# Performance work log

Measured on AMD Instinct MI355X. Metric: run time of the kernel, lower is better.

Reference implementation:

```python
import jax, jax.numpy as jnp
import numpy as np

B, NDOC, L, E = 32, 4, 512, 512
SCALE = np.float32(1.0 / np.sqrt(E))
NEG_INF = np.float32(-1e9)


def setup_inputs() -> dict:
    key = jax.random.key(0)
    k1, k2, k3, k4, k5, k6 = jax.random.split(key, 6)
    return {
        "x1": jax.random.normal(k1, (B, L, E), dtype=jnp.float32),
        "x2": jax.random.normal(k2, (B, NDOC, L, E), dtype=jnp.float32),
        "x1_len": jax.random.randint(k3, (B,), 0, L, dtype=jnp.int64),
        "x2_len": jax.random.randint(k4, (B, NDOC), 0, L, dtype=jnp.int64),
        "fusion_w": jax.random.normal(k5, (2 * E, E), dtype=jnp.float32) * 0.02,
        "fusion_b": jnp.zeros((E,), dtype=jnp.float32),
        "out_w": jax.random.normal(k6, (8 * E, 2 * E), dtype=jnp.float32) * 0.02,
        "out_b": jnp.zeros((2 * E,), dtype=jnp.float32),
    }


def reference(x1, x2, x1_len, x2_len, fusion_w, fusion_b, out_w, out_b):
    # Faithful to torch .repeat(1,4,...): concatenate 4 full copies along batch,
    # so attention row i pairs x1[i % B] with x2[i // 4, i % 4].
    x1_rep = jnp.tile(x1, (NDOC, 1, 1))          # [4B, L, E]
    x2_r = x2.reshape(-1, L, E)                  # [4B, L, E]

    x1_len_r = jnp.tile(x1_len, NDOC)            # [4B] (same tiling as x1_rep)
    x2_len_r = x2_len.reshape(-1)                # [4B]
    pos = jnp.arange(L)
    q_mask = pos[None, :] < x1_len_r[:, None]    # [4B, L]
    k_mask = pos[None, :] < x2_len_r[:, None]    # [4B, L]
    mask = q_mask[:, :, None] & k_mask[:, None, :]  # [4B, L, L]

    # scaled-dot-product attention with masked_fill(mask==0, -1e9)
    scores = jnp.einsum('bqe,bke->bqk', x1_rep, x2_r) * SCALE  # [4B, L, L]
    scores = jnp.where(mask, scores, NEG_INF)
    attn = jax.nn.softmax(scores, axis=-1)
    x1_att = jnp.einsum('bqk,bke->bqe', attn, x2_r)            # [4B, L, E]

    cat = jnp.concatenate([x1_rep - x1_att, x1_rep * x1_att], axis=-1)  # [4B, L, 2E]
    fus = jax.nn.relu(cat @ fusion_w + fusion_b)                        # [4B, L, E]

    x1_mean = jnp.mean(fus, axis=1)              # [4B, E]
    x1_max = jnp.max(fus, axis=1)                # [4B, E]
    pooled = jnp.concatenate([x1_mean.reshape(B, -1), x1_max.reshape(B, -1)], axis=-1)  # [B, 8E]
    out = jax.nn.relu(pooled @ out_w + out_b)    # [B, 2E]
    return out, attn
```

## Files before the change

kernel.cpp:

```cpp
#include <hip/hip_runtime.h>
#include <cstddef>

#define BATCH 32
#define NB    128
#define LL    512
#define EE    512
#define SCALE 0.044194173824159216f
#define NEG_INF -1e9f

typedef __attribute__((ext_vector_type(4))) float f32x4;
typedef __attribute__((ext_vector_type(8))) short s16x8;
typedef __attribute__((ext_vector_type(4))) unsigned short u16x4;

#define STEP_FENCE() asm volatile("s_waitcnt vmcnt(0) lgkmcnt(0)\n\ts_barrier" ::: "memory")

__device__ __forceinline__ unsigned short f2b(float f) {
    unsigned u = __float_as_uint(f);
    u += 0x7FFFu + ((u >> 16) & 1u);
    return (unsigned short)(u >> 16);
}
__device__ __forceinline__ float b2f(unsigned short h) {
    return __uint_as_float(((unsigned)h) << 16);
}

__device__ __forceinline__ void gld_lds16(const unsigned short* g, unsigned short* l) {
    __builtin_amdgcn_global_load_lds(
        (const __attribute__((address_space(1))) void*)g,
        (__attribute__((address_space(3))) void*)l, 16, 0, 0);
}

__global__ __launch_bounds__(256) void k_cvt_x1(
    const float* __restrict__ x1, unsigned short* __restrict__ x1bf)
{
    const size_t idx = (size_t)blockIdx.x * 256 + threadIdx.x;
    f32x4 v = *(const f32x4*)(x1 + idx * 4);
    u16x4 o = { f2b(v[0]), f2b(v[1]), f2b(v[2]), f2b(v[3]) };
    *(u16x4*)(x1bf + idx * 4) = o;
}

__global__ __launch_bounds__(256) void k_cvt_x2(
    const float* __restrict__ x2,
    unsigned short* __restrict__ x2bf, unsigned short* __restrict__ x2t)
{
    __shared__ float T[64][65];
    const int i = blockIdx.z, kb = blockIdx.y * 64, eb = blockIdx.x * 64;
    const float* src = x2 + (size_t)i * LL * EE;
    unsigned short* db = x2bf + (size_t)i * LL * EE;
    unsigned short* dt = x2t  + (size_t)i * LL * EE;
    const int t = threadIdx.x, r16 = t >> 4, c4 = (t & 15) * 4;
#pragma unroll
    for (int p = 0; p < 4; ++p) {
        int row = p * 16 + r16;
        f32x4 v = *(const f32x4*)(src + (size_t)(kb + row) * EE + eb + c4);
        T[row][c4] = v[0]; T[row][c4+1] = v[1]; T[row][c4+2] = v[2]; T[row][c4+3] = v[3];
        u16x4 o = { f2b(v[0]), f2b(v[1]), f2b(v[2]), f2b(v[3]) };
        *(u16x4*)(db + (size_t)(kb + row) * EE + eb + c4) = o;
    }
    __syncthreads();
#pragma unroll
    for (int p = 0; p < 4; ++p) {
        int erow = p * 16 + r16;
        u16x4 o = { f2b(T[c4][erow]), f2b(T[c4+1][erow]),
                    f2b(T[c4+2][erow]), f2b(T[c4+3][erow]) };
        *(u16x4*)(dt + (size_t)(eb + erow) * LL + kb + c4) = o;
    }
}

__global__ __launch_bounds__(256) void k_cvt_fw(
    const float* __restrict__ fw, unsigned short* __restrict__ fwt)
{
    __shared__ float T[64][65];
    const int jb = blockIdx.y * 64, eb = blockIdx.x * 64;
    const int t = threadIdx.x, r16 = t >> 4, c4 = (t & 15) * 4;
#pragma unroll
    for (int p = 0; p < 4; ++p) {
        int row = p * 16 + r16;
        f32x4 v = *(const f32x4*)(fw + (size_t)(jb + row) * EE + eb + c4);
        T[row][c4] = v[0]; T[row][c4+1] = v[1]; T[row][c4+2] = v[2]; T[row][c4+3] = v[3];
    }
    __syncthreads();
#pragma unroll
    for (int p = 0; p < 4; ++p) {
        int erow = p * 16 + r16;
#pragma unroll
        for (int k = 0; k < 4; ++k) {
            int jold = jb + c4 + k;
            int jn = (jold < 512) ? (2 * jold) : (2 * (jold - 512) + 1);
            fwt[(size_t)(eb + erow) * 1024 + jn] = f2b(T[c4 + k][erow]);
        }
    }
}

__global__ __launch_bounds__(1024, 4) void k_attn(
    const unsigned short* __restrict__ x1bf,
    const unsigned short* __restrict__ x2bf,
    const unsigned short* __restrict__ x2t,
    const int* __restrict__ x1_len, const int* __restrict__ x2_len,
    float* __restrict__ attn, unsigned short* __restrict__ Cbuf)
{
    __shared__ __align__(16) char smem[163840];
    unsigned short* Ast0 = (unsigned short*)smem;
    unsigned short* Ast1 = (unsigned short*)(smem + 8192);
    unsigned short* Bst0 = (unsigned short*)(smem + 16384);
    unsigned short* Bst1 = (unsigned short*)(smem + 49152);
    float* rowred = (float*)(smem + 131072);
    float* rowst  = (float*)(smem + 131072 + 4096);
    unsigned short* Vst0 = (unsigned short*)(smem + 131072);
    unsigned short* Vst1 = (unsigned short*)(smem + 147456);

    const int flat = blockIdx.x + blockIdx.y * 128;
    const int xcd  = flat & 7;
    const int idx  = flat >> 3;
    const int i    = xcd * 16 + (idx >> 2);
    const int q0   = (idx & 3) * 128;
    const unsigned short* Ag = x1bf + (size_t)(i & 31) * LL * EE;
    const unsigned short* Bg = x2bf + (size_t)i * LL * EE;
    const unsigned short* Vg = x2t  + (size_t)i * LL * EE;
    const int t = threadIdx.x, lane = t & 63;
    const int w = t >> 6;
    const int m = lane & 15, quad = lane >> 4;
    const int lrow = lane >> 2, lcol = (lane & 3) * 8;
    const int wrow = w >> 3, wcol = w & 7;

    f32x4 acc[4][4];
#pragma unroll
    for (int r = 0; r < 4; ++r)
#pragma unroll
        for (int c = 0; c < 4; ++c) acc[r][c] = (f32x4){0.f, 0.f, 0.f, 0.f};

    if (w < 8)
        gld_lds16(Ag + (size_t)(q0 + w * 16 + lrow) * EE + lcol, &Ast0[w * 512]);
    gld_lds16(Bg + (size_t)((2 * w) * 16 + lrow) * EE + lcol, &Bst0[(2 * w) * 512]);
    gld_lds16(Bg + (size_t)((2 * w + 1) * 16 + lrow) * EE + lcol, &Bst0[(2 * w + 1) * 512]);
    STEP_FENCE();

    for (int it = 0; it < 16; ++it) {
        unsigned short* Ac = (it & 1) ? Ast1 : Ast0;
        unsigned short* Bc = (it & 1) ? Bst1 : Bst0;
        if (it < 15) {
            unsigned short* An = (it & 1) ? Ast0 : Ast1;
            unsigned short* Bn = (it & 1) ? Bst0 : Bst1;
            const int e0n = (it + 1) * 32;
            if (w < 8)
                gld_lds16(Ag + (size_t)(q0 + w * 16 + lrow) * EE + e0n + lcol, &An[w * 512]);
            gld_lds16(Bg + (size_t)((2 * w) * 16 + lrow) * EE + e0n + lcol, &Bn[(2 * w) * 512]);
            gld_lds16(Bg + (size_t)((2 * w + 1) * 16 + lrow) * EE + e0n + lcol, &Bn[(2 * w + 1) * 512]);
        }
        s16x8 af[4], bfr[4];
#pragma unroll
        for (int rt = 0; rt < 4; ++rt)
            af[rt] = *(const s16x8*)&Ac[(wrow * 64 + rt * 16 + m) * 32 + quad * 8];
#pragma unroll
        for (int ct = 0; ct < 4; ++ct)
            bfr[ct] = *(const s16x8*)&Bc[(wcol * 64 + ct * 16 + m) * 32 + quad * 8];
#pragma unroll
        for (int rt = 0; rt < 4; ++rt)
#pragma unroll
            for (int ct = 0; ct < 4; ++ct)
                acc[rt][ct] = __builtin_amdgcn_mfma_f32_16x16x32_bf16(
                    af[rt], bfr[ct], acc[rt][ct], 0, 0, 0);
        STEP_FENCE();
    }

    const int qlen = x1_len[i & 31];
    const int klen = x2_len[i];

#pragma unroll
    for (int rt = 0; rt < 4; ++rt)
#pragma unroll
        for (int reg = 0; reg < 4; ++reg) {
            const int l = q0 + wrow * 64 + rt * 16 + quad * 4 + reg;
            const bool qok = l < qlen;
#pragma unroll
            for (int ct = 0; ct < 4; ++ct) {
                const int k = wcol * 64 + ct * 16 + m;
                acc[rt][ct][reg] = (qok && k < klen) ? acc[rt][ct][reg] * SCALE : NEG_INF;
            }
        }

#pragma unroll
    for (int rt = 0; rt < 4; ++rt)
#pragma unroll
        for (int reg = 0; reg < 4; ++reg) {
            float v = fmaxf(fmaxf(acc[rt][0][reg], acc[rt][1][reg]),
                            fmaxf(acc[rt][2][reg], acc[rt][3][reg]));
            v = fmaxf(v, __shfl_xor(v, 1));
            v = fmaxf(v, __shfl_xor(v, 2));
            v = fmaxf(v, __shfl_xor(v, 4));
            v = fmaxf(v, __shfl_xor(v, 8));
            if (m == 0)
                rowred[wcol * 128 + wrow * 64 + rt * 16 + quad * 4 + reg] = v;
        }
    __syncthreads();
    if (t < 128) {
        float mx = rowred[t];
#pragma unroll
        for (int c = 1; c < 8; ++c) mx = fmaxf(mx, rowred[c * 128 + t]);
        rowst[t] = mx;
    }
    __syncthreads();

#pragma unroll
    for (int rt = 0; rt < 4; ++rt)
#pragma unroll
        for (int reg = 0; reg < 4; ++reg) {
            const int lloc = wrow * 64 + rt * 16 + quad * 4 + reg;
            const float mx = rowst[lloc];
            float s = 0.f;
#pragma unroll
            for (int ct = 0; ct < 4; ++ct) {
                float p = __expf(acc[rt][ct][reg] - mx);
                acc[rt][ct][reg] = p;
                s += p;
            }
            s += __shfl_xor(s, 1);
            s += __shfl_xor(s, 2);
            s += __shfl_xor(s, 4);
            s += __shfl_xor(s, 8);
            if (m == 0) rowred[wcol * 128 + lloc] = s;
        }
    __syncthreads();
    if (t < 128) {
        float s = 0.f;
#pragma unroll
        for (int c = 0; c < 8; ++c) s += rowred[c * 128 + t];
        rowst[t] = 1.0f / s;
    }
    __syncthreads();

    float* op = attn + (size_t)i * LL * LL;
#pragma unroll
    for (int rt = 0; rt < 4; ++rt)
#pragma unroll
        for (int reg = 0; reg < 4; ++reg) {
            const int lloc = wrow * 64 + rt * 16 + quad * 4 + reg;
            const float inv = rowst[lloc];
#pragma unroll
            for (int ct = 0; ct < 4; ++ct) {
                const int k = wcol * 64 + ct * 16 + m;
                float p = acc[rt][ct][reg] * inv;
                op[(size_t)(q0 + lloc) * LL + k] = p;
                unsigned off = (unsigned)(lloc * 1024 + k * 2) ^ (unsigned)((lloc & 7) << 4);
                *(unsigned short*)(smem + off) = f2b(p);
            }
        }
    __syncthreads();

    const int pwr = w >> 2, pwc = w & 3;
    unsigned short* Cb = Cbuf + (size_t)i * LL * 1024;
#pragma unroll
    for (int eh = 0; eh < 2; ++eh) {
        f32x4 acc2[2][4];
#pragma unroll
        for (int r = 0; r < 2; ++r)
#pragma unroll
            for (int c = 0; c < 4; ++c) acc2[r][c] = (f32x4){0.f, 0.f, 0.f, 0.f};

        gld_lds16(Vg + (size_t)(eh * 256 + w * 16 + lrow) * LL + lcol, &Vst0[w * 512]);
        STEP_FENCE();

        for (int kt = 0; kt < 16; ++kt) {
            const int k0 = kt * 32;
            unsigned short* Vc = (kt & 1) ? Vst1 : Vst0;
            if (kt < 15) {
                unsigned short* Vn = (kt & 1) ? Vst0 : Vst1;
                gld_lds16(Vg + (size_t)(eh * 256 + w * 16 + lrow) * LL + k0 + 32 + lcol,
                          &Vn[w * 512]);
            }
            s16x8 paf[2], pbf[4];
#pragma unroll
            for (int rt = 0; rt < 2; ++rt) {
                const int lr = pwr * 32 + rt * 16 + m;
                unsigned off = (unsigned)(lr * 1024 + (k0 + quad * 8) * 2)
                               ^ (unsigned)((lr & 7) << 4);
                paf[rt] = *(const s16x8*)(smem + off);
            }
#pragma unroll
            for (int ct = 0; ct < 4; ++ct)
                pbf[ct] = *(const s16x8*)&Vc[(pwc * 64 + ct * 16 + m) * 32 + quad * 8];
#pragma unroll
            for (int rt = 0; rt < 2; ++rt)
#pragma unroll
                for (int ct = 0; ct < 4; ++ct)
                    acc2[rt][ct] = __builtin_amdgcn_mfma_f32_16x16x32_bf16(
                        paf[rt], pbf[ct], acc2[rt][ct], 0, 0, 0);
            STEP_FENCE();
        }

#pragma unroll
        for (int rt = 0; rt < 2; ++rt)
#pragma unroll
            for (int reg = 0; reg < 4; ++reg) {
                const int l = q0 + pwr * 32 + rt * 16 + quad * 4 + reg;
#pragma unroll
                for (int ct = 0; ct < 4; ++ct) {
                    const int e = eh * 256 + pwc * 64 + ct * 16 + m;
                    float att = acc2[rt][ct][reg];
                    float xv  = b2f(Ag[(size_t)l * EE + e]);
                    unsigned pr = (unsigned)f2b(xv - att) | ((unsigned)f2b(xv * att) << 16);
                    *(unsigned*)(Cb + (size_t)l * 1024 + 2 * e) = pr;
                }
            }
    }
}

__global__ __launch_bounds__(256) void k_fuse_mfma(
    const unsigned short* __restrict__ Cbuf,
    const unsigned short* __restrict__ fwt,
    const float* __restrict__ fb,
    float* __restrict__ pmean, float* __restrict__ pmax)
{
    __shared__ unsigned short Al[128 * 32];
    __shared__ unsigned short Bl[128 * 32];
    __shared__ float psum[2][128];
    __shared__ float pmx[2][128];
    const int i  = blockIdx.x;
    const int lt = blockIdx.y >> 2;
    const int e0 = (blockIdx.y & 3) * 128;
    const unsigned short* Ab = Cbuf + ((size_t)i * LL + lt * 128) * 1024;
    const int t = threadIdx.x, lane = t & 63;
    const int w = t >> 6, wrow = w >> 1, wcol = w & 1;
    const int m = lane & 15, quad = lane >> 4;
    const int lrow = lane >> 2, lcol = (lane & 3) * 8;

    float bias[4];
#pragma unroll
    for (int ct = 0; ct < 4; ++ct) bias[ct] = fb[e0 + wcol * 64 + ct * 16 + m];
    float csum[4] = {0.f, 0.f, 0.f, 0.f};
    float cmax[4] = {-3e38f, -3e38f, -3e38f, -3e38f};

    f32x4 acc[4][4];
#pragma unroll
    for (int r = 0; r < 4; ++r)
#pragma unroll
        for (int c = 0; c < 4; ++c) acc[r][c] = (f32x4){0.f, 0.f, 0.f, 0.f};

    for (int j0 = 0; j0 < 1024; j0 += 32) {
#pragma unroll
        for (int c = 0; c < 2; ++c) {
            const int s = c * 4 + w;
            gld_lds16(Ab + (size_t)(s * 16 + lrow) * 1024 + j0 + lcol, &Al[s * 512]);
            gld_lds16(fwt + (size_t)(e0 + s * 16 + lrow) * 1024 + j0 + lcol, &Bl[s * 512]);
        }
        __syncthreads();
        s16x8 af[4], bfr[4];
#pragma unroll
        for (int rt = 0; rt < 4; ++rt)
            af[rt] = *(const s16x8*)&Al[(wrow * 64 + rt * 16 + m) * 32 + quad * 8];
#pragma unroll
        for (int ct = 0; ct < 4; ++ct)
            bfr[ct] = *(const s16x8*)&Bl[(wcol * 64 + ct * 16 + m) * 32 + quad * 8];
#pragma unroll
        for (int rt = 0; rt < 4; ++rt)
#pragma unroll
            for (int ct = 0; ct < 4; ++ct)
                acc[rt][ct] = __builtin_amdgcn_mfma_f32_16x16x32_bf16(
                    af[rt], bfr[ct], acc[rt][ct], 0, 0, 0);
        __syncthreads();
    }
#pragma unroll
    for (int rt = 0; rt < 4; ++rt)
#pragma unroll
        for (int reg = 0; reg < 4; ++reg)
#pragma unroll
            for (int ct = 0; ct < 4; ++ct) {
                float f = fmaxf(acc[rt][ct][reg] + bias[ct], 0.f);
                csum[ct] += f;
                cmax[ct] = fmaxf(cmax[ct], f);
            }
#pragma unroll
    for (int ct = 0; ct < 4; ++ct) {
        csum[ct] += __shfl_xor(csum[ct], 16);
        csum[ct] += __shfl_xor(csum[ct], 32);
        cmax[ct] = fmaxf(cmax[ct], __shfl_xor(cmax[ct], 16));
        cmax[ct] = fmaxf(cmax[ct], __shfl_xor(cmax[ct], 32));
    }
    if (quad == 0) {
#pragma unroll
        for (int ct = 0; ct < 4; ++ct) {
            psum[wrow][wcol * 64 + ct * 16 + m] = csum[ct];
            pmx[wrow][wcol * 64 + ct * 16 + m] = cmax[ct];
        }
    }
    __syncthreads();
    if (t < 128) {
        float s  = psum[0][t] + psum[1][t];
        float mx = fmaxf(pmx[0][t], pmx[1][t]);
        pmean[((size_t)i * 4 + lt) * EE + e0 + t] = s;
        pmax[((size_t)i * 4 + lt) * EE + e0 + t]  = mx;
    }
}

__global__ __launch_bounds__(256) void k_out_split(
    const float* __restrict__ pmean, const float* __restrict__ pmax,
    const float* __restrict__ ow, float* __restrict__ partial)
{
    __shared__ float ps[256];
    const int kc = blockIdx.x;
    const int b  = blockIdx.y;
    const int t  = threadIdx.x;
    const int j  = kc * 256 + t;
    const int jj = (j < 2048) ? j : j - 2048;
    const int ii = 4 * b + (jj >> 9);
    const int e  = jj & 511;
    float v;
    if (j < 2048) {
        const float* bp = pmean + (size_t)ii * 4 * EE + e;
        v = (bp[0] + bp[512] + bp[1024] + bp[1536]) * (1.0f / 512.0f);
    } else {
        const float* bp = pmax + (size_t)ii * 4 * EE + e;
        v = fmaxf(fmaxf(bp[0], bp[512]), fmaxf(bp[1024], bp[1536]));
    }
    ps[t] = v;
    __syncthreads();
    f32x4 acc = {0.f, 0.f, 0.f, 0.f};
    const float* wp = ow + (size_t)kc * 256 * 1024 + t * 4;
#pragma unroll 8
    for (int q = 0; q < 256; ++q) {
        f32x4 w4 = *(const f32x4*)(wp + (size_t)q * 1024);
        float p = ps[q];
        acc[0] = fmaf(p, w4[0], acc[0]);
        acc[1] = fmaf(p, w4[1], acc[1]);
        acc[2] = fmaf(p, w4[2], acc[2]);
        acc[3] = fmaf(p, w4[3], acc[3]);
    }
    *(f32x4*)(partial + ((size_t)kc * 32 + b) * 1024 + t * 4) = acc;
}

__global__ __launch_bounds__(256) void k_out_final(
    const float* __restrict__ partial, const float* __restrict__ ob,
    float* __restrict__ out)
{
    const int idx = blockIdx.x * 256 + threadIdx.x;
    const int b = idx >> 10, o = idx & 1023;
    float s = ob[o];
#pragma unroll
    for (int kc = 0; kc < 16; ++kc)
        s += partial[((size_t)kc * 32 + b) * 1024 + o];
    out[idx] = fmaxf(s, 0.f);
}

extern "C" void kernel_launch(void* const* d_in, const int* in_sizes, int n_in,
                              void* d_out, int out_size, void* d_ws, size_t ws_size,
                              hipStream_t stream)
{
    const float* x1     = (const float*)d_in[0];
    const float* x2     = (const float*)d_in[1];
    const int*   x1_len = (const int*)d_in[2];
    const int*   x2_len = (const int*)d_in[3];
    const float* fw     = (const float*)d_in[4];
    const float* fb     = (const float*)d_in[5];
    const float* ow     = (const float*)d_in[6];
    const float* ob     = (const float*)d_in[7];

    float* out  = (float*)d_out;
    float* attn = out + (size_t)BATCH * 1024;

    char* wp = (char*)d_ws;
    unsigned short* x1bf   = (unsigned short*)wp; wp += (size_t)BATCH * LL * EE * 2;
    unsigned short* x2bf   = (unsigned short*)wp; wp += (size_t)NB * LL * EE * 2;
    unsigned short* x2t    = (unsigned short*)wp; wp += (size_t)NB * LL * EE * 2;
    unsigned short* Cbuf   = (unsigned short*)wp; wp += (size_t)NB * LL * 1024 * 2;
    unsigned short* fwt    = (unsigned short*)wp; wp += (size_t)EE * 1024 * 2;
    float* pmean   = (float*)wp; wp += (size_t)NB * 4 * EE * 4;
    float* pmax    = (float*)wp; wp += (size_t)NB * 4 * EE * 4;
    float* partial = (float*)wp; wp += (size_t)16 * BATCH * 1024 * 4;

    k_cvt_x1<<<dim3(BATCH * LL * EE / 4 / 256), 256, 0, stream>>>(x1, x1bf);
    k_cvt_x2<<<dim3(8, 8, NB), 256, 0, stream>>>(x2, x2bf, x2t);
    k_cvt_fw<<<dim3(8, 16), 256, 0, stream>>>(fw, fwt);
    k_attn<<<dim3(128, 4), 1024, 0, stream>>>(x1bf, x2bf, x2t, x1_len, x2_len, attn, Cbuf);
    k_fuse_mfma<<<dim3(128, 16), 256, 0, stream>>>(Cbuf, fwt, fb, pmean, pmax);
    k_out_split<<<dim3(16, BATCH), 256, 0, stream>>>(pmean, pmax, ow, partial);
    k_out_final<<<dim3(BATCH * 1024 / 256), 256, 0, stream>>>(partial, ob, out);
}
```

Baseline: 576.7 us.

## Triple-buffer global-to-LDS staging in score and fusion GEMM loops

Replaces the double-buffered load/compute loops in the attention score GEMM and the fusion GEMM with a three-slot ring. Each step waits only for the oldest in-flight loads using partial vmcnt counts and a single barrier per iteration, with loads issued two steps ahead. This is meant to hide global-load latency and drop the second per-step barrier and full drain. In exchange it uses more LDS (three 40 KB slots in k_attn overlap the region later reused for row stats and V, and k_fuse grows to 48 KB). The correctness of the waits depends on the exact per-wave load counts.

```diff
diff --git a/kernel.cpp b/kernel.cpp
--- a/kernel.cpp
+++ b/kernel.cpp
@@ -99,10 +99,6 @@
     float* __restrict__ attn, unsigned short* __restrict__ Cbuf)
 {
     __shared__ __align__(16) char smem[163840];
-    unsigned short* Ast0 = (unsigned short*)smem;
-    unsigned short* Ast1 = (unsigned short*)(smem + 8192);
-    unsigned short* Bst0 = (unsigned short*)(smem + 16384);
-    unsigned short* Bst1 = (unsigned short*)(smem + 49152);
     float* rowred = (float*)(smem + 131072);
     float* rowst  = (float*)(smem + 131072 + 4096);
     unsigned short* Vst0 = (unsigned short*)(smem + 131072);
@@ -128,24 +124,30 @@
 #pragma unroll
         for (int c = 0; c < 4; ++c) acc[r][c] = (f32x4){0.f, 0.f, 0.f, 0.f};
 
-    if (w < 8)
-        gld_lds16(Ag + (size_t)(q0 + w * 16 + lrow) * EE + lcol, &Ast0[w * 512]);
-    gld_lds16(Bg + (size_t)((2 * w) * 16 + lrow) * EE + lcol, &Bst0[(2 * w) * 512]);
-    gld_lds16(Bg + (size_t)((2 * w + 1) * 16 + lrow) * EE + lcol, &Bst0[(2 * w + 1) * 512]);
-    STEP_FENCE();
-
+#define STAGE_SCORES(sl, base)                                                          \
+    do {                                                                                \
+        unsigned short* An_ = (unsigned short*)(base);                                  \
+        unsigned short* Bn_ = (unsigned short*)((char*)(base) + 8192);                  \
+        const int e0_ = (sl) * 32;                                                      \
+        if (w < 8)                                                                      \
+            gld_lds16(Ag + (size_t)(q0 + w * 16 + lrow) * EE + e0_ + lcol, &An_[w * 512]); \
+        gld_lds16(Bg + (size_t)((2 * w) * 16 + lrow) * EE + e0_ + lcol, &Bn_[(2 * w) * 512]); \
+        gld_lds16(Bg + (size_t)((2 * w + 1) * 16 + lrow) * EE + e0_ + lcol, &Bn_[(2 * w + 1) * 512]); \
+    } while (0)
+
+    STAGE_SCORES(0, smem);
+    STAGE_SCORES(1, smem + 40960);
+
+#pragma unroll
     for (int it = 0; it < 16; ++it) {
-        unsigned short* Ac = (it & 1) ? Ast1 : Ast0;
-        unsigned short* Bc = (it & 1) ? Bst1 : Bst0;
-        if (it < 15) {
-            unsigned short* An = (it & 1) ? Ast0 : Ast1;
-            unsigned short* Bn = (it & 1) ? Bst0 : Bst1;
-            const int e0n = (it + 1) * 32;
-            if (w < 8)
-                gld_lds16(Ag + (size_t)(q0 + w * 16 + lrow) * EE + e0n + lcol, &An[w * 512]);
-            gld_lds16(Bg + (size_t)((2 * w) * 16 + lrow) * EE + e0n + lcol, &Bn[(2 * w) * 512]);
-            gld_lds16(Bg + (size_t)((2 * w + 1) * 16 + lrow) * EE + e0n + lcol, &Bn[(2 * w + 1) * 512]);
-        }
+        if (it == 15)   asm volatile("s_waitcnt vmcnt(0)" ::: "memory");
+        else if (w < 8) asm volatile("s_waitcnt vmcnt(3)" ::: "memory");
+        else            asm volatile("s_waitcnt vmcnt(2)" ::: "memory");
+        __builtin_amdgcn_s_barrier();
+        if (it < 14) STAGE_SCORES(it + 2, smem + 40960 * ((it + 2) % 3));
+        char* cb = smem + 40960 * (it % 3);
+        unsigned short* Ac = (unsigned short*)cb;
+        unsigned short* Bc = (unsigned short*)(cb + 8192);
         s16x8 af[4], bfr[4];
 #pragma unroll
         for (int rt = 0; rt < 4; ++rt)
@@ -159,8 +161,8 @@
             for (int ct = 0; ct < 4; ++ct)
                 acc[rt][ct] = __builtin_amdgcn_mfma_f32_16x16x32_bf16(
                     af[rt], bfr[ct], acc[rt][ct], 0, 0, 0);
-        STEP_FENCE();
-    }
+    }
+    __syncthreads();
 
     const int qlen = x1_len[i & 31];
     const int klen = x2_len[i];
@@ -302,6 +304,7 @@
                 }
             }
     }
+#undef STAGE_SCORES
 }
 
 __global__ __launch_bounds__(256) void k_fuse_mfma(
@@ -310,8 +313,7 @@
     const float* __restrict__ fb,
     float* __restrict__ pmean, float* __restrict__ pmax)
 {
-    __shared__ unsigned short Al[128 * 32];
-    __shared__ unsigned short Bl[128 * 32];
+    __shared__ __align__(16) char fsm[49152];
     __shared__ float psum[2][128];
     __shared__ float pmx[2][128];
     const int i  = blockIdx.x;
@@ -335,29 +337,46 @@
 #pragma unroll
         for (int c = 0; c < 4; ++c) acc[r][c] = (f32x4){0.f, 0.f, 0.f, 0.f};
 
-    for (int j0 = 0; j0 < 1024; j0 += 32) {
-#pragma unroll
-        for (int c = 0; c < 2; ++c) {
-            const int s = c * 4 + w;
-            gld_lds16(Ab + (size_t)(s * 16 + lrow) * 1024 + j0 + lcol, &Al[s * 512]);
-            gld_lds16(fwt + (size_t)(e0 + s * 16 + lrow) * 1024 + j0 + lcol, &Bl[s * 512]);
-        }
-        __syncthreads();
+#define STAGE_FUSE(sl, base)                                                            \
+    do {                                                                                \
+        unsigned short* Al_ = (unsigned short*)(base);                                  \
+        unsigned short* Bl_ = (unsigned short*)((char*)(base) + 8192);                  \
+        const int j0_ = (sl) * 32;                                                      \
+        _Pragma("unroll")                                                               \
+        for (int c_ = 0; c_ < 2; ++c_) {                                                \
+            const int s_ = c_ * 4 + w;                                                  \
+            gld_lds16(Ab + (size_t)(s_ * 16 + lrow) * 1024 + j0_ + lcol, &Al_[s_ * 512]); \
+            gld_lds16(fwt + (size_t)(e0 + s_ * 16 + lrow) * 1024 + j0_ + lcol, &Bl_[s_ * 512]); \
+        }                                                                               \
+    } while (0)
+
+    STAGE_FUSE(0, fsm);
+    STAGE_FUSE(1, fsm + 16384);
+
+#pragma unroll
+    for (int it = 0; it < 32; ++it) {
+        if (it == 31) asm volatile("s_waitcnt vmcnt(0)" ::: "memory");
+        else          asm volatile("s_waitcnt vmcnt(4)" ::: "memory");
+        __builtin_amdgcn_s_barrier();
+        if (it < 30) STAGE_FUSE(it + 2, fsm + 16384 * ((it + 2) % 3));
+        char* cb = fsm + 16384 * (it % 3);
+        unsigned short* Ac = (unsigned short*)cb;
+        unsigned short* Bc = (unsigned short*)(cb + 8192);
         s16x8 af[4], bfr[4];
 #pragma unroll
         for (int rt = 0; rt < 4; ++rt)
-            af[rt] = *(const s16x8*)&Al[(wrow * 64 + rt * 16 + m) * 32 + quad * 8];
+            af[rt] = *(const s16x8*)&Ac[(wrow * 64 + rt * 16 + m) * 32 + quad * 8];
 #pragma unroll
         for (int ct = 0; ct < 4; ++ct)
-            bfr[ct] = *(const s16x8*)&Bl[(wcol * 64 + ct * 16 + m) * 32 + quad * 8];
+            bfr[ct] = *(const s16x8*)&Bc[(wcol * 64 + ct * 16 + m) * 32 + quad * 8];
 #pragma unroll
         for (int rt = 0; rt < 4; ++rt)
 #pragma unroll
             for (int ct = 0; ct < 4; ++ct)
                 acc[rt][ct] = __builtin_amdgcn_mfma_f32_16x16x32_bf16(
                     af[rt], bfr[ct], acc[rt][ct], 0, 0, 0);
-        __syncthreads();
-    }
+    }
+#undef STAGE_FUSE
 #pragma unroll
     for (int rt = 0; rt < 4; ++rt)
 #pragma unroll
```

Measured after the change: 548.6 us. 4.9% less time.
